# Kernel tuning notes

Hardware: AMD Instinct MI355X
Metric: run time of the kernel (lower is better)

The kernel has to match this reference:

```python
import jax, jax.numpy as jnp
import numpy as np

DX = 0.005
GAMMA = 1.4


def setup_inputs() -> dict:
    key = jax.random.key(0)
    k1, k2, k3 = jax.random.split(key, 3)
    m, l = 4096, 4096
    rho = 1.0 + jax.random.uniform(k1, (m, 1, l), dtype=jnp.float32)   # density > 0
    vel = 0.1 * jax.random.normal(k2, (m, 1, l), dtype=jnp.float32)
    p = 1.0 + jax.random.uniform(k3, (m, 1, l), dtype=jnp.float32)     # pressure > 0
    mom = rho * vel
    E = p / (GAMMA - 1.0) + 0.5 * rho * vel * vel                      # total energy
    u = jnp.concatenate([rho, mom, E], axis=1)                         # [m, 3, l]
    return {"u": u}


def _prim(w, mm_H=None):
    rho = w[:, 0:1, :]
    mo = w[:, 1:2, :]
    E = w[:, 2:3, :]
    p = (GAMMA - 1.0) * (E - 0.5 * mo * mo / rho)
    H = (E + p) / rho
    return rho, mo, H


def _roe(u):
    # zero-gradient boundary padding (replicate edge cells)
    ul = jnp.concatenate([u[:, :, 0:1], u[:, :, :-1]], axis=2)
    ur = jnp.concatenate([u[:, :, 1:], u[:, :, -1:]], axis=2)

    rm, mm, Hm = _prim(u)
    rr, mr, Hr = _prim(ur)
    rl, ml, Hl = _prim(ul)

    sm = jnp.sqrt(rm)
    sr = jnp.sqrt(rr)
    sl = jnp.sqrt(rl)

    def roe_avg(s_o, m_o, H_o):
        S = s_o + sm
        u_a = (m_o / s_o + mm / sm) / S          # Roe-averaged velocity
        H_a = (s_o * H_o + sm * Hm) / S          # Roe-averaged enthalpy
        c_a = jnp.sqrt((GAMMA - 1.0) * (H_a - 0.5 * u_a * u_a))  # sound speed
        return u_a, H_a, c_a

    u_r, H_r, c_r = roe_avg(sr, mr, Hr)
    u_l, H_l, c_l = roe_avg(sl, ml, Hl)

    def flux_side(u_a, H_a, c_a, du, sign):
        # sign=-1: negative part of eigenvalue (right face); sign=+1: positive part (left face)
        c1 = 0.5 * (GAMMA - 1.0) / (c_a * c_a)
        c2 = 0.5 * u_a * u_a
        c3 = c_a / (GAMMA - 1.0)
        l1 = u_a - c_a
        l2 = u_a
        l3 = u_a + c_a
        d0 = du[:, 0:1, :]
        d1 = du[:, 1:2, :]
        d2 = du[:, 2:3, :]
        L0 = (l1 + sign * jnp.abs(l1)) * c1 * ((c2 + u_a * c3) * d0 - (u_a + c3) * d1 + d2)
        L1 = (l2 + sign * jnp.abs(l2)) * 2 * c1 * ((-c2 + c_a * c3) * d0 + u_a * d1 - d2)
        L2 = (l3 + sign * jnp.abs(l3)) * c1 * ((c2 - u_a * c3) * d0 - (u_a - c3) * d1 + d2)
        R0 = L0 + L1 + L2
        R1 = l1 * L0 + u_a * L1 + l3 * L2
        R2 = (H_a - u_a * c_a) * L0 + c2 * L1 + (H_a + u_a * c_a) * L2
        return jnp.concatenate([R0, R1, R2], axis=1)

    Rur = flux_side(u_r, H_r, c_r, ur - u, -1.0)
    Rul = flux_side(u_l, H_l, c_l, u - ul, 1.0)
    return -(Rur + Rul) / (2.0 * DX)


def reference(u):
    return _roe(u)
```

## Files before the change

### kernel.cpp

```cpp
#include <hip/hip_runtime.h>

#define LROW 4096
#define NT   256
#define EPT  4
#define TILE (NT * EPT)
#define GM1  0.4f

__device__ __forceinline__ float frcp(float x){ return __builtin_amdgcn_rcpf(x); }
__device__ __forceinline__ float frsq(float x){ return __builtin_amdgcn_rsqf(x); }

template<bool RIGHT>
__device__ __forceinline__ void flux_side(
    float s_m, float q_m, float sH_m,
    float s_o, float q_o, float sH_o,
    float d0, float d1, float d2,
    float& R0, float& R1, float& R2)
{
    float rS  = frcp(s_o + s_m);
    float ua  = (q_o + q_m) * rS;
    float Ha  = (sH_o + sH_m) * rS;
    float c2  = 0.5f * ua * ua;
    float ca2 = GM1 * (Ha - c2);
    float rca = frsq(ca2);
    float ca  = ca2 * rca;
    float c1  = (0.5f * GM1) * (rca * rca);
    float c3  = ca * (1.0f / GM1);
    float l1  = ua - ca, l3 = ua + ca;
    float w1  = RIGHT ? fminf(l1, 0.f) : fmaxf(l1, 0.f);
    float w2  = RIGHT ? fminf(ua, 0.f) : fmaxf(ua, 0.f);
    float w3  = RIGHT ? fminf(l3, 0.f) : fmaxf(l3, 0.f);
    float L0  = (2.f * c1) * w1 * ((c2 + ua * c3) * d0 - (ua + c3) * d1 + d2);
    float L1  = (4.f * c1) * w2 * ((ca * c3 - c2) * d0 + ua * d1 - d2);
    float L2  = (2.f * c1) * w3 * ((c2 - ua * c3) * d0 - (ua - c3) * d1 + d2);
    R0 = L0 + L1 + L2;
    R1 = l1 * L0 + ua * L1 + l3 * L2;
    float uc = ua * ca;
    R2 = (Ha - uc) * L0 + c2 * L1 + (Ha + uc) * L2;
}

__global__ __launch_bounds__(NT)
void roe_kernel(const float* __restrict__ u, float* __restrict__ out)
{
    const int t    = threadIdx.x;
    const int base = blockIdx.x * TILE;
    const size_t rowoff = (size_t)blockIdx.y * (3 * LROW);
    const float* pr = u + rowoff;
    const float* pm = pr + LROW;
    const float* pE = pr + 2 * LROW;

    const int j0 = base + EPT * t;
    int jm = (j0 == 0) ? 0 : j0 - 1;
    int jp = (j0 + EPT >= LROW) ? (LROW - 1) : j0 + EPT;

    float4 r4 = *(const float4*)(pr + j0);
    float4 m4 = *(const float4*)(pm + j0);
    float4 E4 = *(const float4*)(pE + j0);

    float rv[6] = {pr[jm], r4.x, r4.y, r4.z, r4.w, pr[jp]};
    float mv[6] = {pm[jm], m4.x, m4.y, m4.z, m4.w, pm[jp]};
    float Ev[6] = {pE[jm], E4.x, E4.y, E4.z, E4.w, pE[jp]};

    float sv[6], qv[6], sHv[6];
#pragma unroll
    for (int k = 0; k < 6; k++) {
        float rs   = frsq(rv[k]);
        float rinv = rs * rs;
        float p    = GM1 * (Ev[k] - 0.5f * mv[k] * mv[k] * rinv);
        float H    = (Ev[k] + p) * rinv;
        sv[k]  = rv[k] * rs;
        qv[k]  = mv[k] * rs;
        sHv[k] = sv[k] * H;
    }

    float o0[4], o1[4], o2[4];
#pragma unroll
    for (int k = 0; k < 4; k++) {
        const int c = k + 1, l = k, r = k + 2;
        float R0r, R1r, R2r, R0l, R1l, R2l;
        flux_side<true >(sv[c], qv[c], sHv[c], sv[r], qv[r], sHv[r],
                         rv[r] - rv[c], mv[r] - mv[c], Ev[r] - Ev[c],
                         R0r, R1r, R2r);
        flux_side<false>(sv[c], qv[c], sHv[c], sv[l], qv[l], sHv[l],
                         rv[c] - rv[l], mv[c] - mv[l], Ev[c] - Ev[l],
                         R0l, R1l, R2l);
        const float SC = -100.0f;
        o0[k] = SC * (R0r + R0l);
        o1[k] = SC * (R1r + R1l);
        o2[k] = SC * (R2r + R2l);
    }

    float* qo = out + rowoff;
    *(float4*)(qo + j0)            = make_float4(o0[0], o0[1], o0[2], o0[3]);
    *(float4*)(qo + LROW + j0)     = make_float4(o1[0], o1[1], o1[2], o1[3]);
    *(float4*)(qo + 2 * LROW + j0) = make_float4(o2[0], o2[1], o2[2], o2[3]);
}

extern "C" void kernel_launch(void* const* d_in, const int* in_sizes, int n_in,
                              void* d_out, int out_size, void* d_ws, size_t ws_size,
                              hipStream_t stream)
{
    const float* u = (const float*)d_in[0];
    float* out = (float*)d_out;
    const int M = in_sizes[0] / (3 * LROW);
    dim3 grid(LROW / TILE, M);
    roe_kernel<<<grid, NT, 0, stream>>>(u, out);
}
```

Before: 322.0 us.

## Share interface Roe computation between neighboring cells and widen per-thread tile

Restructures the kernel so each interface's Roe average, eigenvector projections and wave strengths are computed once and applied to both adjacent cells, using the fact that the positive and negative eigenvalue parts sum to the eigenvalue. Each thread now handles 8 cells instead of 4, so fewer halo loads and fewer redundant interface computations are needed. This roughly halves the transcendental and arithmetic work per cell. The cost is higher register use per thread and fewer threads overall, which lowers occupancy in a memory-bound kernel.

```diff
diff --git a/kernel.cpp b/kernel.cpp
--- a/kernel.cpp
+++ b/kernel.cpp
@@ -2,41 +2,14 @@
 
 #define LROW 4096
 #define NT   256
-#define EPT  4
+#define EPT  8
 #define TILE (NT * EPT)
+#define NC   (EPT + 2)
+#define NI   (EPT + 1)
 #define GM1  0.4f
 
 __device__ __forceinline__ float frcp(float x){ return __builtin_amdgcn_rcpf(x); }
 __device__ __forceinline__ float frsq(float x){ return __builtin_amdgcn_rsqf(x); }
-
-template<bool RIGHT>
-__device__ __forceinline__ void flux_side(
-    float s_m, float q_m, float sH_m,
-    float s_o, float q_o, float sH_o,
-    float d0, float d1, float d2,
-    float& R0, float& R1, float& R2)
-{
-    float rS  = frcp(s_o + s_m);
-    float ua  = (q_o + q_m) * rS;
-    float Ha  = (sH_o + sH_m) * rS;
-    float c2  = 0.5f * ua * ua;
-    float ca2 = GM1 * (Ha - c2);
-    float rca = frsq(ca2);
-    float ca  = ca2 * rca;
-    float c1  = (0.5f * GM1) * (rca * rca);
-    float c3  = ca * (1.0f / GM1);
-    float l1  = ua - ca, l3 = ua + ca;
-    float w1  = RIGHT ? fminf(l1, 0.f) : fmaxf(l1, 0.f);
-    float w2  = RIGHT ? fminf(ua, 0.f) : fmaxf(ua, 0.f);
-    float w3  = RIGHT ? fminf(l3, 0.f) : fmaxf(l3, 0.f);
-    float L0  = (2.f * c1) * w1 * ((c2 + ua * c3) * d0 - (ua + c3) * d1 + d2);
-    float L1  = (4.f * c1) * w2 * ((ca * c3 - c2) * d0 + ua * d1 - d2);
-    float L2  = (2.f * c1) * w3 * ((c2 - ua * c3) * d0 - (ua - c3) * d1 + d2);
-    R0 = L0 + L1 + L2;
-    R1 = l1 * L0 + ua * L1 + l3 * L2;
-    float uc = ua * ca;
-    R2 = (Ha - uc) * L0 + c2 * L1 + (Ha + uc) * L2;
-}
 
 __global__ __launch_bounds__(NT)
 void roe_kernel(const float* __restrict__ u, float* __restrict__ out)
@@ -49,20 +22,23 @@
     const float* pE = pr + 2 * LROW;
 
     const int j0 = base + EPT * t;
-    int jm = (j0 == 0) ? 0 : j0 - 1;
-    int jp = (j0 + EPT >= LROW) ? (LROW - 1) : j0 + EPT;
+    const int jm = (j0 == 0) ? 0 : j0 - 1;
+    const int jp = (j0 + EPT >= LROW) ? (LROW - 1) : j0 + EPT;
 
-    float4 r4 = *(const float4*)(pr + j0);
-    float4 m4 = *(const float4*)(pm + j0);
-    float4 E4 = *(const float4*)(pE + j0);
+    float4 rA = *(const float4*)(pr + j0);
+    float4 rB = *(const float4*)(pr + j0 + 4);
+    float4 mA = *(const float4*)(pm + j0);
+    float4 mB = *(const float4*)(pm + j0 + 4);
+    float4 EA = *(const float4*)(pE + j0);
+    float4 EB = *(const float4*)(pE + j0 + 4);
 
-    float rv[6] = {pr[jm], r4.x, r4.y, r4.z, r4.w, pr[jp]};
-    float mv[6] = {pm[jm], m4.x, m4.y, m4.z, m4.w, pm[jp]};
-    float Ev[6] = {pE[jm], E4.x, E4.y, E4.z, E4.w, pE[jp]};
+    float rv[NC] = {pr[jm], rA.x, rA.y, rA.z, rA.w, rB.x, rB.y, rB.z, rB.w, pr[jp]};
+    float mv[NC] = {pm[jm], mA.x, mA.y, mA.z, mA.w, mB.x, mB.y, mB.z, mB.w, pm[jp]};
+    float Ev[NC] = {pE[jm], EA.x, EA.y, EA.z, EA.w, EB.x, EB.y, EB.z, EB.w, pE[jp]};
 
-    float sv[6], qv[6], sHv[6];
+    float sv[NC], qv[NC], sHv[NC];
 #pragma unroll
-    for (int k = 0; k < 6; k++) {
+    for (int k = 0; k < NC; k++) {
         float rs   = frsq(rv[k]);
         float rinv = rs * rs;
         float p    = GM1 * (Ev[k] - 0.5f * mv[k] * mv[k] * rinv);
@@ -72,27 +48,64 @@
         sHv[k] = sv[k] * H;
     }
 
-    float o0[4], o1[4], o2[4];
+    float o0[EPT], o1[EPT], o2[EPT];
 #pragma unroll
-    for (int k = 0; k < 4; k++) {
-        const int c = k + 1, l = k, r = k + 2;
-        float R0r, R1r, R2r, R0l, R1l, R2l;
-        flux_side<true >(sv[c], qv[c], sHv[c], sv[r], qv[r], sHv[r],
-                         rv[r] - rv[c], mv[r] - mv[c], Ev[r] - Ev[c],
-                         R0r, R1r, R2r);
-        flux_side<false>(sv[c], qv[c], sHv[c], sv[l], qv[l], sHv[l],
-                         rv[c] - rv[l], mv[c] - mv[l], Ev[c] - Ev[l],
-                         R0l, R1l, R2l);
-        const float SC = -100.0f;
-        o0[k] = SC * (R0r + R0l);
-        o1[k] = SC * (R1r + R1l);
-        o2[k] = SC * (R2r + R2l);
+    for (int k = 0; k < EPT; k++) { o0[k] = 0.f; o1[k] = 0.f; o2[k] = 0.f; }
+
+#pragma unroll
+    for (int k = 0; k < NI; k++) {
+        const float d0 = rv[k+1] - rv[k];
+        const float d1 = mv[k+1] - mv[k];
+        const float d2 = Ev[k+1] - Ev[k];
+
+        const float rS  = frcp(sv[k] + sv[k+1]);
+        const float ua  = (qv[k]  + qv[k+1])  * rS;
+        const float Ha  = (sHv[k] + sHv[k+1]) * rS;
+        const float c2  = 0.5f * ua * ua;
+        const float ca2 = GM1 * (Ha - c2);
+        const float rca = frsq(ca2);
+        const float ca  = ca2 * rca;
+        const float k1  = GM1 * (rca * rca);
+        const float c3  = ca * (1.0f / GM1);
+        const float tt  = ua * c3;
+        const float p0  = c2 + tt, q0 = c2 - tt;
+        const float p1  = ua + c3, q1 = ua - c3;
+        const float h2  = fmaf(-ua, ua, Ha);
+
+        const float a0 = k1 * (fmaf(p0, d0, d2) - p1 * d1);
+        const float a1 = (k1 + k1) * fmaf(h2, d0, fmaf(ua, d1, -d2));
+        const float a2 = k1 * (fmaf(q0, d0, d2) - q1 * d1);
+
+        const float l1 = ua - ca, l3 = ua + ca;
+        const float uc = ua * ca;
+        const float Hm = Ha - uc, Hp = Ha + uc;
+        const float w1n = fminf(l1, 0.f);
+        const float w2n = fminf(ua, 0.f);
+        const float w3n = fminf(l3, 0.f);
+
+        if (k >= 1) {
+            const float L0 = w1n * a0, L1 = w2n * a1, L2 = w3n * a2;
+            o0[k-1] += L0 + L1 + L2;
+            o1[k-1] += l1 * L0 + ua * L1 + l3 * L2;
+            o2[k-1] += Hm * L0 + c2 * L1 + Hp * L2;
+        }
+        if (k <= EPT - 1) {
+            const float w1p = l1 - w1n, w2p = ua - w2n, w3p = l3 - w3n;
+            const float L0 = w1p * a0, L1 = w2p * a1, L2 = w3p * a2;
+            o0[k] += L0 + L1 + L2;
+            o1[k] += l1 * L0 + ua * L1 + l3 * L2;
+            o2[k] += Hm * L0 + c2 * L1 + Hp * L2;
+        }
     }
 
+    const float SC = -100.0f;
     float* qo = out + rowoff;
-    *(float4*)(qo + j0)            = make_float4(o0[0], o0[1], o0[2], o0[3]);
-    *(float4*)(qo + LROW + j0)     = make_float4(o1[0], o1[1], o1[2], o1[3]);
-    *(float4*)(qo + 2 * LROW + j0) = make_float4(o2[0], o2[1], o2[2], o2[3]);
+    *(float4*)(qo + j0)     = make_float4(SC*o0[0], SC*o0[1], SC*o0[2], SC*o0[3]);
+    *(float4*)(qo + j0 + 4) = make_float4(SC*o0[4], SC*o0[5], SC*o0[6], SC*o0[7]);
+    *(float4*)(qo + LROW + j0)     = make_float4(SC*o1[0], SC*o1[1], SC*o1[2], SC*o1[3]);
+    *(float4*)(qo + LROW + j0 + 4) = make_float4(SC*o1[4], SC*o1[5], SC*o1[6], SC*o1[7]);
+    *(float4*)(qo + 2*LROW + j0)     = make_float4(SC*o2[0], SC*o2[1], SC*o2[2], SC*o2[3]);
+    *(float4*)(qo + 2*LROW + j0 + 4) = make_float4(SC*o2[4], SC*o2[5], SC*o2[6], SC*o2[7]);
 }
 
 extern "C" void kernel_launch(void* const* d_in, const int* in_sizes, int n_in,
```

Result: no change. 326.1 us (+1.3%).
